# Optimization experiments

Hardware: AMD Instinct MI355X
Metric: run time of the kernel (lower is better)

Reference implementation:

```python
import jax, jax.numpy as jnp
import numpy as np

D_MODEL = 512
N_HEADS = 8
D_K = D_MODEL // N_HEADS


def setup_inputs() -> dict:
    key = jax.random.key(0)
    ks = jax.random.split(key, 12)
    B, L = 2, 512
    s = 1.0 / np.sqrt(D_MODEL)
    sk = 1.0 / np.sqrt(D_K)
    return {
        "query": jax.random.normal(ks[0], (B, L, D_MODEL), jnp.float32),
        "key": jax.random.normal(ks[1], (B, L, D_MODEL), jnp.float32),
        "value": jax.random.normal(ks[2], (B, L, D_MODEL), jnp.float32),
        "Wq": jax.random.normal(ks[3], (D_MODEL, D_MODEL), jnp.float32) * s,
        "bq": jnp.zeros((D_MODEL,), jnp.float32),
        "Wk": jax.random.normal(ks[4], (D_MODEL, D_MODEL), jnp.float32) * s,
        "bk": jnp.zeros((D_MODEL,), jnp.float32),
        "Wv": jax.random.normal(ks[5], (D_MODEL, D_MODEL), jnp.float32) * s,
        "bv": jnp.zeros((D_MODEL,), jnp.float32),
        "Wo": jax.random.normal(ks[6], (D_MODEL, D_MODEL), jnp.float32) * s,
        "bo": jnp.zeros((D_MODEL,), jnp.float32),
        "Aq": jax.random.normal(ks[7], (D_K, D_K), jnp.float32) * sk,  # inner W_q (no bias)
        "Ak": jax.random.normal(ks[8], (D_K, D_K), jnp.float32) * sk,  # inner W_k (no bias)
        "av": jax.random.normal(ks[9], (D_K,), jnp.float32) * sk,      # inner v (d_k -> 1)
    }


def _split_heads(x):
    B, L, _ = x.shape
    return x.reshape(B, L, N_HEADS, D_K).transpose(0, 2, 1, 3)  # [B,H,L,dk]


def reference(query, key, value, Wq, bq, Wk, bk, Wv, bv, Wo, bo, Aq, Ak, av):
    # outer projections (torch Linear: x @ W.T + b)
    Q = _split_heads(query @ Wq.T + bq)   # [B,H,Lq,dk]
    K = _split_heads(key @ Wk.T + bk)     # [B,H,Lk,dk]
    V = _split_heads(value @ Wv.T + bv)   # [B,H,Lk,dk]
    # inner additive attention: e_ij = v^T tanh(Aq q_i + Ak k_j)
    qp = Q @ Aq.T                          # [B,H,Lq,dk]
    kp = K @ Ak.T                          # [B,H,Lk,dk]
    energy = jnp.tanh(qp[:, :, :, None, :] + kp[:, :, None, :, :])  # [B,H,Lq,Lk,dk]
    scores = jnp.einsum('bhqkd,d->bhqk', energy, av)
    attn = jax.nn.softmax(scores, axis=-1)  # dropout disabled (eval)
    out = jnp.einsum('bhqk,bhkd->bhqd', attn, V)  # [B,H,Lq,dk]
    B, _, Lq, _ = out.shape
    out = out.transpose(0, 2, 1, 3).reshape(B, Lq, D_MODEL)
    return out @ Wo.T + bo
```

## Files before the change

### kernel.cpp

```cpp
#include <hip/hip_runtime.h>

#define LOG2E 1.4426950408889634f

typedef __bf16 bf16x8 __attribute__((ext_vector_type(8)));
typedef float f32x4 __attribute__((ext_vector_type(4)));

__device__ __forceinline__ unsigned short bfb(__bf16 b){
  union { __bf16 b; unsigned short u; } z; z.b = b; return z.u;
}
__device__ __forceinline__ void split8(const float* p, bf16x8& hi, bf16x8& lo){
  #pragma unroll
  for (int j = 0; j < 8; j++){
    float f = p[j];
    __bf16 h = (__bf16)f;
    hi[j] = h;
    lo[j] = (__bf16)(f - (float)h);
  }
}


__global__ __launch_bounds__(256) void prep_all(
    const float* __restrict__ Wq, const float* __restrict__ Aq,
    const float* __restrict__ Wk, const float* __restrict__ Ak,
    const float* __restrict__ bq, const float* __restrict__ bk,
    const float* __restrict__ av,
    const float* __restrict__ Wv, const float* __restrict__ Wo,
    unsigned short* __restrict__ W2qp, unsigned short* __restrict__ W2kp,
    unsigned short* __restrict__ Wvp,  unsigned short* __restrict__ Wop,
    float* __restrict__ b2q, float* __restrict__ b2k, float* __restrict__ av2g){
  if (blockIdx.x >= 1024){
    if (blockIdx.x == 1280){
      if (blockIdx.y == 0){
        #pragma unroll
        for (int rep = 0; rep < 2; rep++){
          int n = rep * 256 + threadIdx.x;
          int h = n >> 6, e = n & 63;
          float aq = 0.f, ak = 0.f;
          for (int c = 0; c < 64; c++){
            aq += Aq[e*64 + c] * bq[h*64 + c];
            ak += Ak[e*64 + c] * bk[h*64 + c];
          }
          b2q[n] = aq * (2.f * LOG2E);
          b2k[n] = ak * (2.f * LOG2E);
        }
      } else {
        if (threadIdx.x < 64) av2g[threadIdx.x] = -2.f * LOG2E * av[threadIdx.x];
      }
      return;
    }
    const float* src = blockIdx.y ? Wo : Wv;
    unsigned short* dst = blockIdx.y ? Wop : Wvp;
    int base = ((blockIdx.x - 1024) * 256 + threadIdx.x) * 4;
    int n = base >> 9, k0 = base & 511;
    float4 v = *(const float4*)(src + base);
    ushort4 h, l;
    float f; __bf16 hb;
    f = v.x; hb = (__bf16)f; h.x = bfb(hb); l.x = bfb((__bf16)(f - (float)hb));
    f = v.y; hb = (__bf16)f; h.y = bfb(hb); l.y = bfb((__bf16)(f - (float)hb));
    f = v.z; hb = (__bf16)f; h.z = bfb(hb); l.z = bfb((__bf16)(f - (float)hb));
    f = v.w; hb = (__bf16)f; h.w = bfb(hb); l.w = bfb((__bf16)(f - (float)hb));
    int nt = n >> 4, ln = n & 15;
    int ks = k0 >> 5, q = (k0 & 31) >> 3, j0 = k0 & 7;
    size_t off = (size_t)((nt*16 + ks) * 2) * 512 + (q*16 + ln) * 8 + j0;
    *(ushort4*)(dst + off)       = h;
    *(ushort4*)(dst + off + 512) = l;
    return;
  }
  const float* W  = blockIdx.y ? Wk : Wq;
  const float* Am = blockIdx.y ? Ak : Aq;
  unsigned short* dst = blockIdx.y ? W2kp : W2qp;
  int idx = blockIdx.x * 256 + threadIdx.x;
  int n = idx >> 9, k = idx & 511;
  int h = n >> 6, e = n & 63;
  float acc = 0.f;
  #pragma unroll 8
  for (int c = 0; c < 64; c++)
    acc += Am[e*64 + c] * W[(h*64 + c)*512 + k];
  float v = acc * (2.f * LOG2E);
  __bf16 hb = (__bf16)v;
  int nt = n >> 4, ln = n & 15;
  int ks = k >> 5, q = (k & 31) >> 3, j = k & 7;
  size_t off = (size_t)((nt*16 + ks) * 2) * 512 + (q*16 + ln) * 8 + j;
  dst[off]       = bfb(hb);
  dst[off + 512] = bfb((__bf16)(v - (float)hb));
}

struct GemmBatch {
  const float* Af;
  const unsigned short* Bp;
  const float* bias;
  float* Cf;
  int transposed;
  int expout;
};
struct GemmArgs { GemmBatch g[3]; };

__global__ __launch_bounds__(256) void gemm_nk(GemmArgs ga){
  GemmBatch gb = ga.g[blockIdx.z];
  __shared__ float As[64 * 68];
  const int tid = threadIdx.x, lane = tid & 63, w = tid >> 6;
  const int l15 = lane & 15, quad = lane >> 4;
  const int m0  = blockIdx.x * 64;
  const int nt0 = blockIdx.y * 4;
  f32x4 ac0 = {0.f,0.f,0.f,0.f}, ac1 = ac0, ac2 = ac0, ac3 = ac0;

  const int sr = tid >> 2;
  const int sc = (tid & 3) * 16;
  const float* srcA = gb.Af + (size_t)(m0 + sr) * 512 + sc;
  float* dstA = &As[sr * 68 + sc];

  for (int kc = 0; kc < 8; kc++){
    __syncthreads();
    #pragma unroll
    for (int i = 0; i < 4; i++)
      *(f32x4*)(dstA + i*4) = *(const f32x4*)(srcA + kc*64 + i*4);
    __syncthreads();
    #pragma unroll
    for (int s = 0; s < 2; s++){
      int ks = kc * 2 + s;
      bf16x8 ah, al;
      split8(&As[(w*16 + l15) * 68 + s*32 + quad*8], ah, al);
      #pragma unroll
      for (int t = 0; t < 4; t++){
        const unsigned short* bp = gb.Bp + (size_t)(((nt0 + t)*16 + ks) * 2) * 512 + lane*8;
        bf16x8 bh = *(const bf16x8*)bp;
        bf16x8 bl = *(const bf16x8*)(bp + 512);
        f32x4& ac = (t==0)?ac0:(t==1)?ac1:(t==2)?ac2:ac3;
        ac = __builtin_amdgcn_mfma_f32_16x16x32_bf16(ah, bh, ac, 0, 0, 0);
        ac = __builtin_amdgcn_mfma_f32_16x16x32_bf16(al, bh, ac, 0, 0, 0);
        ac = __builtin_amdgcn_mfma_f32_16x16x32_bf16(ah, bl, ac, 0, 0, 0);
      }
    }
  }

  const int mrow = m0 + w * 16 + quad * 4;
  #pragma unroll
  for (int t = 0; t < 4; t++){
    f32x4 v = (t==0)?ac0:(t==1)?ac1:(t==2)?ac2:ac3;
    int n = nt0 * 16 + t * 16 + l15;
    float bs = gb.bias[n];
    #pragma unroll
    for (int r = 0; r < 4; r++){
      float val = v[r] + bs;
      if (gb.expout) val = __builtin_amdgcn_exp2f(val);
      int m2 = mrow + r;
      if (gb.transposed){
        gb.Cf[(size_t)(((m2 >> 9) * 8 + (n >> 6)) * 64 + (n & 63)) * 512 + (m2 & 511)] = val;
      } else {
        gb.Cf[(size_t)m2 * 512 + n] = val;
      }
    }
  }
}

__global__ __launch_bounds__(512, 4) void attn_kernel(
    const float* __restrict__ eqT, const float* __restrict__ ekp,
    const float* __restrict__ Vv, const float* __restrict__ av2g,
    float* __restrict__ Oh){
  __shared__ float bufA[64 * 130];
  __shared__ float bufB[64 * 130];
  __shared__ unsigned short pcb[2 * 16 * 136];
  __shared__ float dn[16];
  float* cmb = bufA;

  const int tid = threadIdx.x, lane = tid & 63, w = tid >> 6;
  const int l15 = lane & 15, quad = lane >> 4;
  const int bh = blockIdx.y;
  const int i0 = blockIdx.x * 16;
  const size_t kbase = (size_t)(bh >> 3) * 512 * 512 + (size_t)(bh & 7) * 64;
  const int r0 = __builtin_amdgcn_readfirstlane(2 * w);
  const size_t qbase = (size_t)bh * 64 * 512 + i0 + r0;
  const int ntile = w & 3, khalf = w >> 2;

  float den0 = 0.f, den1 = 0.f;
  f32x4 Cacc = {0.f, 0.f, 0.f, 0.f};

  {
    #pragma unroll
    for (int m = 0; m < 8; m++){
      int i = w + 8 * m;
      float a = ekp[kbase + (size_t)(2*i    ) * 512 + lane];
      float b = ekp[kbase + (size_t)(2*i + 1) * 512 + lane];
      *(float2*)&bufA[lane * 130 + 2*i] = make_float2(a, b);
    }
  }
  __syncthreads();

  for (int c = 0; c < 4; c++){
    float va[8], vb[8];
    #pragma unroll
    for (int m = 0; m < 8; m++){
      int i = w + 8 * m;
      va[m] = Vv[kbase + (size_t)(c*128 + 2*i    ) * 512 + lane];
      vb[m] = Vv[kbase + (size_t)(c*128 + 2*i + 1) * 512 + lane];
    }
    float s00 = 0.f, s01 = 0.f, s10 = 0.f, s11 = 0.f;
    #pragma unroll 4
    for (int d = 0; d < 64; d++){
      float2 eq = *(const float2*)(eqT + qbase + (size_t)d * 512);
      float a2 = av2g[d];
      float2 ek = *(const float2*)&bufA[d * 130 + 2 * lane];
      s00 += a2 * __builtin_amdgcn_rcpf(__builtin_fmaf(eq.x, ek.x, 1.f));
      s01 += a2 * __builtin_amdgcn_rcpf(__builtin_fmaf(eq.x, ek.y, 1.f));
      s10 += a2 * __builtin_amdgcn_rcpf(__builtin_fmaf(eq.y, ek.x, 1.f));
      s11 += a2 * __builtin_amdgcn_rcpf(__builtin_fmaf(eq.y, ek.y, 1.f));
    }
    float e00 = __builtin_amdgcn_exp2f(s00);
    float e01 = __builtin_amdgcn_exp2f(s01);
    float e10 = __builtin_amdgcn_exp2f(s10);
    float e11 = __builtin_amdgcn_exp2f(s11);
    den0 += e00 + e01; den1 += e10 + e11;
    {
      __bf16 h00 = (__bf16)e00, h01 = (__bf16)e01, h10 = (__bf16)e10, h11 = (__bf16)e11;
      ushort2 hi0 = { bfb(h00), bfb(h01) };
      ushort2 hi1 = { bfb(h10), bfb(h11) };
      ushort2 lo0 = { bfb((__bf16)(e00 - (float)h00)), bfb((__bf16)(e01 - (float)h01)) };
      ushort2 lo1 = { bfb((__bf16)(e10 - (float)h10)), bfb((__bf16)(e11 - (float)h11)) };
      *(ushort2*)&pcb[(0*16 + r0    ) * 136 + 2*lane] = hi0;
      *(ushort2*)&pcb[(0*16 + r0 + 1) * 136 + 2*lane] = hi1;
      *(ushort2*)&pcb[(1*16 + r0    ) * 136 + 2*lane] = lo0;
      *(ushort2*)&pcb[(1*16 + r0 + 1) * 136 + 2*lane] = lo1;
    }
    #pragma unroll
    for (int m = 0; m < 8; m++){
      int i = w + 8 * m;
      *(float2*)&bufB[lane * 130 + 2*i] = make_float2(va[m], vb[m]);
    }
    __syncthreads();

    float ka[8], kb[8];
    if (c < 3){
      #pragma unroll
      for (int m = 0; m < 8; m++){
        int i = w + 8 * m;
        ka[m] = ekp[kbase + (size_t)((c+1)*128 + 2*i    ) * 512 + lane];
        kb[m] = ekp[kbase + (size_t)((c+1)*128 + 2*i + 1) * 512 + lane];
      }
    }
    #pragma unroll
    for (int kk2 = 0; kk2 < 2; kk2++){
      int k0 = (khalf * 2 + kk2) * 32 + quad * 8;
      bf16x8 ph = *(const bf16x8*)&pcb[(0*16 + l15) * 136 + k0];
      bf16x8 pl = *(const bf16x8*)&pcb[(1*16 + l15) * 136 + k0];
      const float* vp = &bufB[(ntile*16 + l15) * 130 + k0];
      bf16x8 vh, vl;
      #pragma unroll
      for (int j = 0; j < 8; j++){
        float f = vp[j];
        __bf16 h = (__bf16)f;
        vh[j] = h; vl[j] = (__bf16)(f - (float)h);
      }
      Cacc = __builtin_amdgcn_mfma_f32_16x16x32_bf16(ph, vh, Cacc, 0, 0, 0);
      Cacc = __builtin_amdgcn_mfma_f32_16x16x32_bf16(pl, vh, Cacc, 0, 0, 0);
      Cacc = __builtin_amdgcn_mfma_f32_16x16x32_bf16(ph, vl, Cacc, 0, 0, 0);
    }
    if (c < 3){
      #pragma unroll
      for (int m = 0; m < 8; m++){
        int i = w + 8 * m;
        *(float2*)&bufA[lane * 130 + 2*i] = make_float2(ka[m], kb[m]);
      }
    }
    __syncthreads();
  }

  #pragma unroll
  for (int off = 1; off < 64; off <<= 1){
    den0 += __shfl_xor(den0, off, 64);
    den1 += __shfl_xor(den1, off, 64);
  }
  if (lane == 0){ dn[r0] = den0; dn[r0 + 1] = den1; }
  __syncthreads();
  if (w >= 4){
    #pragma unroll
    for (int r = 0; r < 4; r++) cmb[(w - 4) * 256 + lane * 4 + r] = Cacc[r];
  }
  __syncthreads();
  if (w < 4){
    #pragma unroll
    for (int r = 0; r < 4; r++){
      float cv = Cacc[r] + cmb[w * 256 + lane * 4 + r];
      int row = quad * 4 + r;
      int d = ntile * 16 + l15;
      Oh[kbase + (size_t)(i0 + row) * 512 + d] = cv / dn[row];
    }
  }
}

extern "C" void kernel_launch(void* const* d_in, const int* in_sizes, int n_in,
                              void* d_out, int out_size, void* d_ws, size_t ws_size,
                              hipStream_t stream){
  const float* q_in = (const float*)d_in[0];
  const float* k_in = (const float*)d_in[1];
  const float* v_in = (const float*)d_in[2];
  const float* Wq_  = (const float*)d_in[3];
  const float* bq_  = (const float*)d_in[4];
  const float* Wk_  = (const float*)d_in[5];
  const float* bk_  = (const float*)d_in[6];
  const float* Wv_  = (const float*)d_in[7];
  const float* bv_  = (const float*)d_in[8];
  const float* Wo_  = (const float*)d_in[9];
  const float* bo_  = (const float*)d_in[10];
  const float* Aq_  = (const float*)d_in[11];
  const float* Ak_  = (const float*)d_in[12];
  const float* av_  = (const float*)d_in[13];

  char* ws = (char*)d_ws;
  unsigned short* W2qp = (unsigned short*)(ws + 0);
  unsigned short* W2kp = (unsigned short*)(ws + 1048576);
  float* Oh = (float*)(ws + 0);
  unsigned short* Wvp = (unsigned short*)(ws + 2097152);
  unsigned short* Wop = (unsigned short*)(ws + 3145728);
  float* b2q  = (float*)(ws + 4194304);
  float* b2k  = (float*)(ws + 4196352);
  float* av2g = (float*)(ws + 4198400);
  float* eqT  = (float*)(ws + 4198656);
  float* ekp  = (float*)(ws + 6295808);
  float* Vw   = (float*)(ws + 8392960);

  prep_all<<<dim3(1281, 2, 1), 256, 0, stream>>>(Wq_, Aq_, Wk_, Ak_, bq_, bk_, av_,
                                                 Wv_, Wo_,
                                                 W2qp, W2kp, Wvp, Wop,
                                                 b2q, b2k, av2g);

  GemmArgs ga;
  ga.g[0] = { q_in, W2qp, b2q, eqT, 1, 1 };
  ga.g[1] = { k_in, W2kp, b2k, ekp, 0, 1 };
  ga.g[2] = { v_in, Wvp,  bv_, Vw,  0, 0 };
  gemm_nk<<<dim3(16, 8, 3), 256, 0, stream>>>(ga);

  attn_kernel<<<dim3(32, 16, 1), 512, 0, stream>>>(eqT, ekp, Vw, av2g, Oh);

  GemmArgs go;
  go.g[0] = { Oh, Wop, bo_, (float*)d_out, 0, 0 };
  go.g[1] = go.g[0];
  go.g[2] = go.g[0];
  gemm_nk<<<dim3(16, 8, 1), 256, 0, stream>>>(go);
}
```

Before: 170.8 us.

## Double attention block to 1024 threads with one query row per wave

The attention kernel now launches 16 waves per block instead of 8. Each wave computes scores for a single query row rather than two, and the P·V MFMA reduction is split four ways over k instead of two, followed by a three-way partial-sum combine. One barrier before the final combine is also removed. The aim is more waves in flight per CU to hide LDS and global latency, at the cost of less per-thread ILP, more reduction traffic through shared memory, and a tight register budget from the new launch bounds (1024, 8).

```diff
diff --git a/kernel.cpp b/kernel.cpp
--- a/kernel.cpp
+++ b/kernel.cpp
@@ -153,7 +153,7 @@
   }
 }
 
-__global__ __launch_bounds__(512, 4) void attn_kernel(
+__global__ __launch_bounds__(1024, 8) void attn_kernel(
     const float* __restrict__ eqT, const float* __restrict__ ekp,
     const float* __restrict__ Vv, const float* __restrict__ av2g,
     float* __restrict__ Oh){
@@ -168,17 +168,17 @@
   const int bh = blockIdx.y;
   const int i0 = blockIdx.x * 16;
   const size_t kbase = (size_t)(bh >> 3) * 512 * 512 + (size_t)(bh & 7) * 64;
-  const int r0 = __builtin_amdgcn_readfirstlane(2 * w);
+  const int r0 = __builtin_amdgcn_readfirstlane(w);
   const size_t qbase = (size_t)bh * 64 * 512 + i0 + r0;
-  const int ntile = w & 3, khalf = w >> 2;
-
-  float den0 = 0.f, den1 = 0.f;
+  const int ntile = w & 3, kq = w >> 2;
+
+  float den = 0.f;
   f32x4 Cacc = {0.f, 0.f, 0.f, 0.f};
 
   {
     #pragma unroll
-    for (int m = 0; m < 8; m++){
-      int i = w + 8 * m;
+    for (int m = 0; m < 4; m++){
+      int i = w + 16 * m;
       float a = ekp[kbase + (size_t)(2*i    ) * 512 + lane];
       float b = ekp[kbase + (size_t)(2*i + 1) * 512 + lane];
       *(float2*)&bufA[lane * 130 + 2*i] = make_float2(a, b);
@@ -187,59 +187,50 @@
   __syncthreads();
 
   for (int c = 0; c < 4; c++){
-    float va[8], vb[8];
-    #pragma unroll
-    for (int m = 0; m < 8; m++){
-      int i = w + 8 * m;
+    float va[4], vb[4];
+    #pragma unroll
+    for (int m = 0; m < 4; m++){
+      int i = w + 16 * m;
       va[m] = Vv[kbase + (size_t)(c*128 + 2*i    ) * 512 + lane];
       vb[m] = Vv[kbase + (size_t)(c*128 + 2*i + 1) * 512 + lane];
     }
-    float s00 = 0.f, s01 = 0.f, s10 = 0.f, s11 = 0.f;
+    float s0 = 0.f, s1 = 0.f;
     #pragma unroll 4
     for (int d = 0; d < 64; d++){
-      float2 eq = *(const float2*)(eqT + qbase + (size_t)d * 512);
+      float eq = eqT[qbase + (size_t)d * 512];
       float a2 = av2g[d];
       float2 ek = *(const float2*)&bufA[d * 130 + 2 * lane];
-      s00 += a2 * __builtin_amdgcn_rcpf(__builtin_fmaf(eq.x, ek.x, 1.f));
-      s01 += a2 * __builtin_amdgcn_rcpf(__builtin_fmaf(eq.x, ek.y, 1.f));
-      s10 += a2 * __builtin_amdgcn_rcpf(__builtin_fmaf(eq.y, ek.x, 1.f));
-      s11 += a2 * __builtin_amdgcn_rcpf(__builtin_fmaf(eq.y, ek.y, 1.f));
-    }
-    float e00 = __builtin_amdgcn_exp2f(s00);
-    float e01 = __builtin_amdgcn_exp2f(s01);
-    float e10 = __builtin_amdgcn_exp2f(s10);
-    float e11 = __builtin_amdgcn_exp2f(s11);
-    den0 += e00 + e01; den1 += e10 + e11;
+      s0 += a2 * __builtin_amdgcn_rcpf(__builtin_fmaf(eq, ek.x, 1.f));
+      s1 += a2 * __builtin_amdgcn_rcpf(__builtin_fmaf(eq, ek.y, 1.f));
+    }
+    float e0 = __builtin_amdgcn_exp2f(s0);
+    float e1 = __builtin_amdgcn_exp2f(s1);
+    den += e0 + e1;
     {
-      __bf16 h00 = (__bf16)e00, h01 = (__bf16)e01, h10 = (__bf16)e10, h11 = (__bf16)e11;
-      ushort2 hi0 = { bfb(h00), bfb(h01) };
-      ushort2 hi1 = { bfb(h10), bfb(h11) };
-      ushort2 lo0 = { bfb((__bf16)(e00 - (float)h00)), bfb((__bf16)(e01 - (float)h01)) };
-      ushort2 lo1 = { bfb((__bf16)(e10 - (float)h10)), bfb((__bf16)(e11 - (float)h11)) };
-      *(ushort2*)&pcb[(0*16 + r0    ) * 136 + 2*lane] = hi0;
-      *(ushort2*)&pcb[(0*16 + r0 + 1) * 136 + 2*lane] = hi1;
-      *(ushort2*)&pcb[(1*16 + r0    ) * 136 + 2*lane] = lo0;
-      *(ushort2*)&pcb[(1*16 + r0 + 1) * 136 + 2*lane] = lo1;
-    }
-    #pragma unroll
-    for (int m = 0; m < 8; m++){
-      int i = w + 8 * m;
+      __bf16 h0 = (__bf16)e0, h1 = (__bf16)e1;
+      ushort2 hi = { bfb(h0), bfb(h1) };
+      ushort2 lo = { bfb((__bf16)(e0 - (float)h0)), bfb((__bf16)(e1 - (float)h1)) };
+      *(ushort2*)&pcb[(0*16 + r0) * 136 + 2*lane] = hi;
+      *(ushort2*)&pcb[(1*16 + r0) * 136 + 2*lane] = lo;
+    }
+    #pragma unroll
+    for (int m = 0; m < 4; m++){
+      int i = w + 16 * m;
       *(float2*)&bufB[lane * 130 + 2*i] = make_float2(va[m], vb[m]);
     }
     __syncthreads();
 
-    float ka[8], kb[8];
+    float ka[4], kb[4];
     if (c < 3){
       #pragma unroll
-      for (int m = 0; m < 8; m++){
-        int i = w + 8 * m;
+      for (int m = 0; m < 4; m++){
+        int i = w + 16 * m;
         ka[m] = ekp[kbase + (size_t)((c+1)*128 + 2*i    ) * 512 + lane];
         kb[m] = ekp[kbase + (size_t)((c+1)*128 + 2*i + 1) * 512 + lane];
       }
     }
-    #pragma unroll
-    for (int kk2 = 0; kk2 < 2; kk2++){
-      int k0 = (khalf * 2 + kk2) * 32 + quad * 8;
+    {
+      int k0 = kq * 32 + quad * 8;
       bf16x8 ph = *(const bf16x8*)&pcb[(0*16 + l15) * 136 + k0];
       bf16x8 pl = *(const bf16x8*)&pcb[(1*16 + l15) * 136 + k0];
       const float* vp = &bufB[(ntile*16 + l15) * 130 + k0];
@@ -256,8 +247,8 @@
     }
     if (c < 3){
       #pragma unroll
-      for (int m = 0; m < 8; m++){
-        int i = w + 8 * m;
+      for (int m = 0; m < 4; m++){
+        int i = w + 16 * m;
         *(float2*)&bufA[lane * 130 + 2*i] = make_float2(ka[m], kb[m]);
       }
     }
@@ -265,21 +256,20 @@
   }
 
   #pragma unroll
-  for (int off = 1; off < 64; off <<= 1){
-    den0 += __shfl_xor(den0, off, 64);
-    den1 += __shfl_xor(den1, off, 64);
-  }
-  if (lane == 0){ dn[r0] = den0; dn[r0 + 1] = den1; }
+  for (int off = 1; off < 64; off <<= 1)
+    den += __shfl_xor(den, off, 64);
+  if (lane == 0) dn[r0] = den;
+  if (kq > 0){
+    #pragma unroll
+    for (int r = 0; r < 4; r++) cmb[(w - 4) * 256 + lane * 4 + r] = Cacc[r];
+  }
   __syncthreads();
-  if (w >= 4){
-    #pragma unroll
-    for (int r = 0; r < 4; r++) cmb[(w - 4) * 256 + lane * 4 + r] = Cacc[r];
-  }
-  __syncthreads();
-  if (w < 4){
+  if (kq == 0){
     #pragma unroll
     for (int r = 0; r < 4; r++){
-      float cv = Cacc[r] + cmb[w * 256 + lane * 4 + r];
+      float cv = Cacc[r];
+      #pragma unroll
+      for (int j = 0; j < 3; j++) cv += cmb[(j*4 + ntile) * 256 + lane * 4 + r];
       int row = quad * 4 + r;
       int d = ntile * 16 + l15;
       Oh[kbase + (size_t)(i0 + row) * 512 + d] = cv / dn[row];
@@ -329,7 +319,7 @@
   ga.g[2] = { v_in, Wvp,  bv_, Vw,  0, 0 };
   gemm_nk<<<dim3(16, 8, 3), 256, 0, stream>>>(ga);
 
-  attn_kernel<<<dim3(32, 16, 1), 512, 0, stream>>>(eqT, ekp, Vw, av2g, Oh);
+  attn_kernel<<<dim3(32, 16, 1), 1024, 0, stream>>>(eqT, ekp, Vw, av2g, Oh);
 
   GemmArgs go;
   go.g[0] = { Oh, Wop, bo_, (float*)d_out, 0, 0 };
```

Measured after the change: 168.7 us. Within noise of the previous version (-1.2%).
